# Kernel optimization log

Measured on AMD Instinct MI355X. Metric: run time of the kernel, lower is better.

## Reference

```python
import jax, jax.numpy as jnp
import numpy as np

# Complete K-ary forest: B trees, depth D levels, BFS node numbering per tree.
B, K, D = 64, 4, 6
V, L = 600, 256
N_PER = (K ** D - 1) // (K - 1)   # 1365 nodes per tree
N = B * N_PER                      # 87360 total nodes


def _schedule():
    """Per-(depth, sibling_index) groups, mirroring the torch decode_train loop
    for a complete K-ary forest. Returns list of (d, s, node_idx, parent_idx)."""
    starts = [(K ** d - 1) // (K - 1) for d in range(D)]  # level offsets within a tree
    tree_off = np.arange(B)[:, None] * N_PER
    groups = []
    for d in range(D):
        for s in (range(1) if d == 0 else range(K)):
            if d == 0:
                p = np.arange(1)                      # root
                par = None
            else:
                p = np.arange(K ** (d - 1)) * K + s   # positions with sib_pos == s
                par = (tree_off + starts[d - 1] + (p // K)[None, :]).reshape(-1)
            idx = (tree_off + starts[d] + p[None, :]).reshape(-1)
            groups.append((d, s, jnp.asarray(idx),
                           None if par is None else jnp.asarray(par)))
    return groups

GROUPS = _schedule()


def _lstm(gx, h, c, W_hh, b_ih, b_hh):
    # torch LSTMCell, gate order i, f, g, o; gx = x @ W_ih^T precomputed.
    gates = gx + b_ih + h @ W_hh.T + b_hh
    i, f, g, o = jnp.split(gates, 4, axis=1)
    c_new = jax.nn.sigmoid(f) * c + jax.nn.sigmoid(i) * jnp.tanh(g)
    return jax.nn.sigmoid(o) * jnp.tanh(c_new), c_new


def setup_inputs() -> dict:
    key = jax.random.key(0)
    ks = jax.random.split(key, 20)
    w = lambda k, shape, s=0.05: jax.random.normal(k, shape, dtype=jnp.float32) * s
    return {
        'z': w(ks[0], (B, L), 1.0),
        'features': jax.random.randint(ks[1], (N,), 0, V),
        'W_ih_p': w(ks[2], (4 * L, V)), 'W_hh_p': w(ks[3], (4 * L, L)),
        'b_ih_p': w(ks[4], (4 * L,)), 'b_hh_p': w(ks[5], (4 * L,)),
        'W_ih_s': w(ks[6], (4 * L, V)), 'W_hh_s': w(ks[7], (4 * L, L)),
        'b_ih_s': w(ks[8], (4 * L,)), 'b_hh_s': w(ks[9], (4 * L,)),
        'U_parent': w(ks[10], (L, L)), 'U_sibling': w(ks[11], (L, L)),
        'W_label': w(ks[12], (V, L)), 'b_label': w(ks[13], (V,)),
        'W_depth': w(ks[14], (1, L)), 'b_depth': w(ks[15], (1,)),
        'W_width': w(ks[16], (1, L)), 'b_width': w(ks[17], (1,)),
        'w_off_p': w(ks[18], (1, 1), 1.0), 'w_off_s': w(ks[19], (1, 1), 1.0),
    }


def reference(z, features, W_ih_p, W_hh_p, b_ih_p, b_hh_p,
              W_ih_s, W_hh_s, b_ih_s, b_hh_s, U_parent, U_sibling,
              W_label, b_label, W_depth, b_depth, W_width, b_width,
              w_off_p, w_off_s):
    h_p = jnp.zeros((N, L), jnp.float32)
    c_p = jnp.zeros((N, L), jnp.float32)
    h_s = jnp.zeros((N, L), jnp.float32)
    c_s = jnp.zeros((N, L), jnp.float32)
    pred_labels = jnp.zeros((N, V), jnp.float32)
    pred_is_parent = jnp.zeros((N,), jnp.float32)
    pred_has_sib = jnp.zeros((N,), jnp.float32)

    for d, s, idx, pidx in GROUPS:
        G = idx.shape[0]
        if d == 0:
            h_par, c_par = z, jnp.zeros((B, L), jnp.float32)
        else:
            h_par, c_par = h_p[pidx], c_p[pidx]
        if s == 0:
            h_prev = jnp.zeros((G, L), jnp.float32)
            c_prev = jnp.zeros((G, L), jnp.float32)
        else:
            h_prev, c_prev = h_s[idx - 1], c_s[idx - 1]
        # group-constant teacher flags for a complete K-ary tree
        is_par = 1.0 if d < D - 1 else 0.0
        has_sib = 1.0 if (d > 0 and s < K - 1) else 0.0

        h_pred = jnp.tanh(h_par @ U_parent.T + h_prev @ U_sibling.T)
        logits = h_pred @ W_label.T + b_label
        p_par = jax.nn.sigmoid(h_pred @ W_depth.T + b_depth)[:, 0]
        p_sib = jax.nn.sigmoid(h_pred @ W_width.T + b_width)[:, 0]
        logp = jax.nn.log_softmax(
            logits + w_off_p[0, 0] * is_par + w_off_s[0, 0] * has_sib, axis=1)

        lab = features[idx]
        gx_p = jnp.take(W_ih_p, lab, axis=1).T  # one-hot @ W_ih^T as a gather
        gx_s = jnp.take(W_ih_s, lab, axis=1).T
        hp_new, cp_new = _lstm(gx_p, h_par, c_par, W_hh_p, b_ih_p, b_hh_p)
        hs_new, cs_new = _lstm(gx_s, h_prev, c_prev, W_hh_s, b_ih_s, b_hh_s)

        h_p = h_p.at[idx].set(hp_new)
        c_p = c_p.at[idx].set(cp_new)
        h_s = h_s.at[idx].set(hs_new)
        c_s = c_s.at[idx].set(cs_new)
        pred_labels = pred_labels.at[idx].set(logp)
        pred_is_parent = pred_is_parent.at[idx].set(p_par)
        pred_has_sib = pred_has_sib.at[idx].set(p_sib)

    # pack [N, V+2]: log-softmax labels, p(is_parent), p(has_sibling)
    return jnp.concatenate(
        [pred_labels, pred_is_parent[:, None], pred_has_sib[:, None]], axis=1)
```

## Files before the change

### kernel.cpp

```cpp
#include <hip/hip_runtime.h>


typedef unsigned short u16;
typedef short bf16x8 __attribute__((ext_vector_type(8)));
typedef float f32x4 __attribute__((ext_vector_type(4)));

#define NPER 1365
#define VDIM 600
#define VD2  602

#define MODE_PPA   0
#define MODE_UPROJ 1
#define MODE_ROOT  2

__device__ __forceinline__ float b2f(u16 h) {
  union { unsigned u; float f; } v; v.u = ((unsigned)h) << 16; return v.f;
}
__device__ __forceinline__ u16 f2bf(float f) {
  union { float f; unsigned u; } v; v.f = f;
  unsigned r = v.u + 0x7fff + ((v.u >> 16) & 1);
  return (u16)(r >> 16);
}
__device__ __forceinline__ float fsigm(float x) {
  return __fdividef(1.f, 1.f + __expf(-x));
}
__device__ __forceinline__ float ftanh(float x) {
  float e = __expf(-2.f * fabsf(x));
  float r = __fdividef(1.f - e, 1.f + e);
  return x < 0.f ? -r : r;
}

__device__ __forceinline__ void ladder(int r, int& off, int& pcs, int& start) {
  if (r < 64)        { off = 0;    pcs = 0; start = 1;   }
  else if (r < 320)  { off = 64;   pcs = 2; start = 5;   }
  else if (r < 1344) { off = 320;  pcs = 4; start = 21;  }
  else if (r < 5440) { off = 1344; pcs = 6; start = 85;  }
  else               { off = 5440; pcs = 8; start = 341; }
}

__global__ void k_pack(
    const float* __restrict__ Upar, const float* __restrict__ Whhp,
    const float* __restrict__ Usib, const float* __restrict__ Whhs,
    const float* __restrict__ z, const float* __restrict__ Wihp,
    const float* __restrict__ Wihs, const float* __restrict__ Wlab,
    const float* __restrict__ Wd, const float* __restrict__ Ww,
    const float* __restrict__ blab, const float* __restrict__ bd,
    const float* __restrict__ bw, const float* __restrict__ bihp,
    const float* __restrict__ bhhp, const float* __restrict__ bihs,
    const float* __restrict__ bhhs,
    u16* __restrict__ UPWHHP, u16* __restrict__ USWHHS, u16* __restrict__ ZBF,
    u16* __restrict__ WIHPT, u16* __restrict__ WIHST, u16* __restrict__ WEXT,
    float* __restrict__ BE, float* __restrict__ BP, float* __restrict__ BS) {
  int i = blockIdx.x * 256 + threadIdx.x;
  if (i < 327680) {
    int r = i >> 8, c = i & 255;
    UPWHHP[i] = f2bf(r < 256 ? Upar[(r << 8) | c] : Whhp[((r - 256) << 8) | c]);
    return;
  }
  i -= 327680;
  if (i < 327680) {
    int r = i >> 8, c = i & 255;
    USWHHS[i] = f2bf(r < 256 ? Usib[(r << 8) | c] : Whhs[((r - 256) << 8) | c]);
    return;
  }
  i -= 327680;
  if (i < 16384) { ZBF[i] = f2bf(z[i]); return; }
  i -= 16384;
  if (i < 614400) {
    int r = i >> 10, c = i & 1023;
    WIHPT[i] = f2bf(Wihp[c * VDIM + r]); return;
  }
  i -= 614400;
  if (i < 614400) {
    int r = i >> 10, c = i & 1023;
    WIHST[i] = f2bf(Wihs[c * VDIM + r]); return;
  }
  i -= 614400;
  if (i < VD2 * 256) {
    int r = i >> 8, c = i & 255;
    float v = (r < VDIM) ? Wlab[r * 256 + c] : ((r == VDIM) ? Wd[c] : Ww[c]);
    WEXT[i] = f2bf(v); return;
  }
  i -= VD2 * 256;
  if (i < VD2) { BE[i] = (i < VDIM) ? blab[i] : ((i == VDIM) ? bd[0] : bw[0]); return; }
  i -= VD2;
  if (i < 1024) { BP[i] = bihp[i] + bhhp[i]; return; }
  i -= 1024;
  if (i < 1024) { BS[i] = bihs[i] + bhhs[i]; return; }
}

__device__ __forceinline__ void dev_dual(
    int tile, int nx, const u16* __restrict__ A, const u16* __restrict__ B,
    int M, int mode, u16* __restrict__ ppa, int ppoff,
    float* __restrict__ uproj, u16* __restrict__ gates,
    u16* __restrict__ hpred) {
  static __shared__ __align__(16) u16 As[128 * 40];
  static __shared__ __align__(16) u16 Bs[128 * 40];
  const int m0 = (tile % nx) * 128, n0 = (tile / nx) * 128;
  const int tid = threadIdx.x;
  const int wave = tid >> 6, lane = tid & 63;
  const int quad = lane >> 4, lr = lane & 15;
  const int wm = (wave >> 1) * 64, wn = (wave & 1) * 64;
  const int srow = tid >> 2;
  const int sch = (tid & 3) << 3;

  f32x4 acc[4][4] = {};
  for (int t = 0; t < 8; ++t) {
    const int kk = t * 32;
    bf16x8 a0 = *(const bf16x8*)(A + (size_t)(m0 + srow) * 256 + kk + sch);
    bf16x8 a1 = *(const bf16x8*)(A + (size_t)(m0 + srow + 64) * 256 + kk + sch);
    bf16x8 b0 = *(const bf16x8*)(B + (size_t)(n0 + srow) * 256 + kk + sch);
    bf16x8 b1 = *(const bf16x8*)(B + (size_t)(n0 + srow + 64) * 256 + kk + sch);
    __syncthreads();
    *(bf16x8*)&As[srow * 40 + sch] = a0;
    *(bf16x8*)&As[(srow + 64) * 40 + sch] = a1;
    *(bf16x8*)&Bs[srow * 40 + sch] = b0;
    *(bf16x8*)&Bs[(srow + 64) * 40 + sch] = b1;
    __syncthreads();
    bf16x8 af[4], bfr[4];
#pragma unroll
    for (int tm = 0; tm < 4; ++tm)
      af[tm] = *(const bf16x8*)&As[(wm + tm * 16 + lr) * 40 + quad * 8];
#pragma unroll
    for (int tn = 0; tn < 4; ++tn)
      bfr[tn] = *(const bf16x8*)&Bs[(wn + tn * 16 + lr) * 40 + quad * 8];
#pragma unroll
    for (int tm = 0; tm < 4; ++tm)
#pragma unroll
      for (int tn = 0; tn < 4; ++tn)
        acc[tm][tn] = __builtin_amdgcn_mfma_f32_16x16x32_bf16(
            af[tm], bfr[tn], acc[tm][tn], 0, 0, 0);
  }

  const bool isg = (n0 >= 256);
#pragma unroll
  for (int tn = 0; tn < 4; ++tn) {
    int col = n0 + wn + tn * 16 + lr;
#pragma unroll
    for (int tm = 0; tm < 4; ++tm) {
#pragma unroll
      for (int r = 0; r < 4; ++r) {
        int row = m0 + wm + tm * 16 + quad * 4 + r;
        if (row >= M) continue;
        float v = acc[tm][tn][r];
        if (isg) {
          gates[(size_t)row * 1024 + (col - 256)] = f2bf(v);
        } else if (mode == MODE_PPA) {
          ppa[(size_t)(ppoff + row) * 256 + col] = f2bf(v);
        } else if (mode == MODE_UPROJ) {
          uproj[(size_t)row * 256 + col] = v;
        } else {
          hpred[(size_t)row * NPER * 256 + col] = f2bf(ftanh(v));
        }
      }
    }
  }
}


__device__ __forceinline__ void dev_s0(int r, const u16* __restrict__ wihT,
    const float* __restrict__ bias, const int* __restrict__ feat,
    u16* __restrict__ h, u16* __restrict__ c) {
  int u = threadIdx.x;
  int off, pcs, start; ladder(r, off, pcs, start);
  int lg = r - off;
  int t = lg >> pcs, j = lg & ((1 << pcs) - 1);
  int lab = feat[t * NPER + start + 4 * j];
  const u16* wr = wihT + lab * 1024;
  float gi = b2f(wr[u])       + bias[u];
  float gg = b2f(wr[512 + u]) + bias[512 + u];
  float go = b2f(wr[768 + u]) + bias[768 + u];
  float cn = fsigm(gi) * ftanh(gg);
  float hn = fsigm(go) * ftanh(cn);
  h[(size_t)r * 256 + u] = f2bf(hn);
  c[(size_t)r * 256 + u] = f2bf(cn);
}

__device__ __forceinline__ void dev_lstm_sib(int r, int k,
    const u16* __restrict__ gates, const u16* __restrict__ wihT,
    const float* __restrict__ bias, const u16* __restrict__ c_in,
    const int* __restrict__ feat, u16* __restrict__ h, u16* __restrict__ c) {
  int u = threadIdx.x;
  int off, pcs, start; ladder(r, off, pcs, start);
  int lg = r - off;
  int t = lg >> pcs, j = lg & ((1 << pcs) - 1);
  int lab = feat[t * NPER + start + 4 * j + k];
  const u16* wr = wihT + lab * 1024;
  const u16* gr = gates + (size_t)r * 1024;
  float gi = b2f(wr[u])       + bias[u]       + b2f(gr[u]);
  float gf = b2f(wr[256 + u]) + bias[256 + u] + b2f(gr[256 + u]);
  float gg = b2f(wr[512 + u]) + bias[512 + u] + b2f(gr[512 + u]);
  float go = b2f(wr[768 + u]) + bias[768 + u] + b2f(gr[768 + u]);
  float cv = b2f(c_in[(size_t)r * 256 + u]);
  float cn = fsigm(gf) * cv + fsigm(gi) * ftanh(gg);
  float hn = fsigm(go) * ftanh(cn);
  h[(size_t)r * 256 + u] = f2bf(hn);
  c[(size_t)r * 256 + u] = f2bf(cn);
}

__device__ __forceinline__ void dev_lstm_par(int g,
    const u16* __restrict__ gates, const u16* __restrict__ wihT,
    const float* __restrict__ bias, const u16* __restrict__ c_in,
    const int* __restrict__ feat, u16* __restrict__ h, u16* __restrict__ c,
    int lsbits, int start) {
  int u = threadIdx.x;
  int t = g >> lsbits, p = g & ((1 << lsbits) - 1);
  int pr = lsbits ? ((t << (lsbits - 2)) | (p >> 2)) : g;
  int lab = feat[t * NPER + start + p];
  const u16* wr = wihT + lab * 1024;
  const u16* gr = gates + (size_t)pr * 1024;
  float gi = b2f(wr[u])       + bias[u]       + b2f(gr[u]);
  float gf = b2f(wr[256 + u]) + bias[256 + u] + b2f(gr[256 + u]);
  float gg = b2f(wr[512 + u]) + bias[512 + u] + b2f(gr[512 + u]);
  float go = b2f(wr[768 + u]) + bias[768 + u] + b2f(gr[768 + u]);
  float cv = c_in ? b2f(c_in[(size_t)pr * 256 + u]) : 0.f;
  float cn = fsigm(gf) * cv + fsigm(gi) * ftanh(gg);
  float hn = fsigm(go) * ftanh(cn);
  h[(size_t)g * 256 + u] = f2bf(hn);
  c[(size_t)g * 256 + u] = f2bf(cn);
}

__device__ __forceinline__ void dev_assemble(int r,
    const u16* __restrict__ PPA, const float* __restrict__ U1,
    const float* __restrict__ U2, const float* __restrict__ U3,
    u16* __restrict__ HPRED) {
  int u = threadIdx.x;
  int off, pcs, start; ladder(r, off, pcs, start);
  int lg = r - off;
  int t = lg >> pcs, j = lg & ((1 << pcs) - 1);
  size_t base = ((size_t)(t * NPER + start + 4 * j)) * 256 + u;
  size_t ro = (size_t)r * 256 + u;
  float pp = b2f(PPA[ro]);
  HPRED[base]       = f2bf(ftanh(pp));
  HPRED[base + 256] = f2bf(ftanh(pp + U1[ro]));
  HPRED[base + 512] = f2bf(ftanh(pp + U2[ro]));
  HPRED[base + 768] = f2bf(ftanh(pp + U3[ro]));
}


__global__ __launch_bounds__(256) void k_s0(
    const u16* WIHST, const float* BS, const int* feat, u16* h, u16* c) {
  dev_s0(blockIdx.x, WIHST, BS, feat, h, c);
}

__global__ __launch_bounds__(256) void k_gg(
    int nA,
    const u16* Aa, const u16* Ba, int Ma, int nxa, int modea,
    u16* ppaa, int ppoffa, float* uproja, u16* gatesa, u16* hpreda,
    const u16* Ab, const u16* Bb, int Mb, int nxb, int modeb,
    u16* ppab, int ppoffb, float* uprojb, u16* gatesb, u16* hpredb) {
  int b = blockIdx.x;
  if (b < nA)
    dev_dual(b, nxa, Aa, Ba, Ma, modea, ppaa, ppoffa, uproja, gatesa, hpreda);
  else
    dev_dual(b - nA, nxb, Ab, Bb, Mb, modeb, ppab, ppoffb, uprojb, gatesb,
             hpredb);
}

__global__ __launch_bounds__(256) void k_gemm(
    const u16* A, const u16* B, int M, int nx, int mode,
    u16* ppa, int ppoff, float* uproj, u16* gates, u16* hpred) {
  dev_dual(blockIdx.x, nx, A, B, M, mode, ppa, ppoff, uproj, gates, hpred);
}

__global__ __launch_bounds__(256) void k_ll(
    int nP,
    const u16* gatesP, const u16* WIHPT, const float* BP, const u16* cpin,
    u16* hpout, u16* cpout, int lsbits, int startp,
    int kS, const u16* gatesS, const u16* WIHST, const float* BS,
    const u16* csin, u16* hsout, u16* csout, const int* feat) {
  int b = blockIdx.x;
  if (b < nP)
    dev_lstm_par(b, gatesP, WIHPT, BP, cpin, feat, hpout, cpout, lsbits,
                 startp);
  else
    dev_lstm_sib(b - nP, kS, gatesS, WIHST, BS, csin, feat, hsout, csout);
}

__global__ __launch_bounds__(256) void k_plstm(
    const u16* gatesP, const u16* WIHPT, const float* BP, const u16* cpin,
    const int* feat, u16* hpout, u16* cpout, int lsbits, int start) {
  dev_lstm_par(blockIdx.x, gatesP, WIHPT, BP, cpin, feat, hpout, cpout,
               lsbits, start);
}

__global__ __launch_bounds__(256) void k_plstm_asm(
    const u16* gatesP, const u16* WIHPT, const float* BP, const u16* cpin,
    const int* feat, u16* hpout, u16* cpout,
    const u16* PPA, const float* U1, const float* U2, const float* U3,
    u16* HPRED) {
  int b = blockIdx.x;
  if (b < 16384)
    dev_lstm_par(b, gatesP, WIHPT, BP, cpin, feat, hpout, cpout, 8, 85);
  else
    dev_assemble(b - 16384, PPA, U1, U2, U3, HPRED);
}

__global__ __launch_bounds__(256) void k_assemble(
    const u16* PPA, const float* U1, const float* U2, const float* U3,
    u16* HPRED) {
  dev_assemble(5440 + blockIdx.x, PPA, U1, U2, U3, HPRED);
}

__global__ __launch_bounds__(512, 4) void k_mm_tail(
    const u16* __restrict__ A, const u16* __restrict__ B,
    const float* __restrict__ bias, float* __restrict__ out) {
  __shared__ __align__(16) u16 As[32 * 264];
  __shared__ float smax[32][8], ssum[32][8], slz[32];
  const int m0 = blockIdx.x * 32;
  const int tid = threadIdx.x;
  const int wave = tid >> 6, lane = tid & 63;
  const int quad = lane >> 4, lr = lane & 15;
  const int c0 = wave * 80;

#pragma unroll
  for (int c = 0; c < 2; ++c) {
    int idx = c * 512 + tid;
    int row = idx >> 5, ch = (idx & 31) << 3;
    *(bf16x8*)&As[row * 264 + ch] =
        *(const bf16x8*)(A + (size_t)(m0 + row) * 256 + ch);
  }
  __syncthreads();

  f32x4 acc[2][5] = {};
#pragma unroll
  for (int t = 0; t < 8; ++t) {
    bf16x8 af[2], bfr[5];
#pragma unroll
    for (int tm = 0; tm < 2; ++tm)
      af[tm] = *(const bf16x8*)&As[(tm * 16 + lr) * 264 + t * 32 + quad * 8];
#pragma unroll
    for (int tn = 0; tn < 5; ++tn)
      bfr[tn] = *(const bf16x8*)(B + (size_t)(c0 + tn * 16 + lr) * 256 +
                                 t * 32 + quad * 8);
#pragma unroll
    for (int tm = 0; tm < 2; ++tm)
#pragma unroll
      for (int tn = 0; tn < 5; ++tn)
        acc[tm][tn] = __builtin_amdgcn_mfma_f32_16x16x32_bf16(
            af[tm], bfr[tn], acc[tm][tn], 0, 0, 0);
  }

  float bv[5]; bool val[5];
#pragma unroll
  for (int tn = 0; tn < 5; ++tn) {
    int col = c0 + tn * 16 + lr;
    val[tn] = (col < VDIM);
    bv[tn] = (col < VD2) ? bias[col] : 0.f;
  }

#pragma unroll
  for (int tm = 0; tm < 2; ++tm) {
#pragma unroll
    for (int r = 0; r < 4; ++r) {
      float mx = -1e30f;
#pragma unroll
      for (int tn = 0; tn < 5; ++tn)
        if (val[tn]) mx = fmaxf(mx, acc[tm][tn][r] + bv[tn]);
#pragma unroll
      for (int o = 1; o < 16; o <<= 1) mx = fmaxf(mx, __shfl_xor(mx, o, 64));
      if (lr == 0) smax[tm * 16 + quad * 4 + r][wave] = mx;
    }
  }
  __syncthreads();
#pragma unroll
  for (int tm = 0; tm < 2; ++tm) {
#pragma unroll
    for (int r = 0; r < 4; ++r) {
      int row = tm * 16 + quad * 4 + r;
      float fm = smax[row][0];
#pragma unroll
      for (int wv = 1; wv < 8; ++wv) fm = fmaxf(fm, smax[row][wv]);
      float se = 0.f;
#pragma unroll
      for (int tn = 0; tn < 5; ++tn)
        if (val[tn]) se += __expf(acc[tm][tn][r] + bv[tn] - fm);
#pragma unroll
      for (int o = 1; o < 16; o <<= 1) se += __shfl_xor(se, o, 64);
      if (lr == 0) ssum[row][wave] = se;
    }
  }
  __syncthreads();
  if (tid < 32) {
    float fm = smax[tid][0];
#pragma unroll
    for (int wv = 1; wv < 8; ++wv) fm = fmaxf(fm, smax[tid][wv]);
    float ss = 0.f;
#pragma unroll
    for (int wv = 0; wv < 8; ++wv) ss += ssum[tid][wv];
    slz[tid] = fm + __logf(ss);
  }
  __syncthreads();

#pragma unroll
  for (int tm = 0; tm < 2; ++tm) {
#pragma unroll
    for (int tn = 0; tn < 5; ++tn) {
      int col = c0 + tn * 16 + lr;
      if (col >= VD2) continue;
#pragma unroll
      for (int r = 0; r < 4; ++r) {
        int row = tm * 16 + quad * 4 + r;
        float v = acc[tm][tn][r] + bv[tn];
        out[(size_t)(m0 + row) * VD2 + col] =
            (col < VDIM) ? (v - slz[row]) : fsigm(v);
      }
    }
  }
}


extern "C" void kernel_launch(void* const* d_in, const int* in_sizes, int n_in,
                              void* d_out, int out_size, void* d_ws, size_t ws_size,
                              hipStream_t stream) {
  const float* z    = (const float*)d_in[0];
  const int*   feat = (const int*)d_in[1];
  const float* Wihp = (const float*)d_in[2];
  const float* Whhp = (const float*)d_in[3];
  const float* bihp = (const float*)d_in[4];
  const float* bhhp = (const float*)d_in[5];
  const float* Wihs = (const float*)d_in[6];
  const float* Whhs = (const float*)d_in[7];
  const float* bihs = (const float*)d_in[8];
  const float* bhhs = (const float*)d_in[9];
  const float* Upar = (const float*)d_in[10];
  const float* Usib = (const float*)d_in[11];
  const float* Wlab = (const float*)d_in[12];
  const float* blab = (const float*)d_in[13];
  const float* Wd   = (const float*)d_in[14];
  const float* bd   = (const float*)d_in[15];
  const float* Ww   = (const float*)d_in[16];
  const float* bw   = (const float*)d_in[17];
  float* out = (float*)d_out;

  char* w = (char*)d_ws;
  auto alloc = [&](size_t bytes) {
    char* p = w; w += (bytes + 255) & ~(size_t)255; return p;
  };
  u16*   UPWHHP = (u16*)alloc((size_t)1280 * 256 * 2);
  u16*   USWHHS = (u16*)alloc((size_t)1280 * 256 * 2);
  u16*   ZBF    = (u16*)alloc((size_t)128 * 256 * 2);
  u16*   WIHPT  = (u16*)alloc((size_t)VDIM * 1024 * 2);
  u16*   WIHST  = (u16*)alloc((size_t)VDIM * 1024 * 2);
  u16*   WEXT   = (u16*)alloc((size_t)640 * 256 * 2);
  float* BE     = (float*)alloc(VD2 * 4);
  float* BP     = (float*)alloc(1024 * 4);
  float* BS     = (float*)alloc(1024 * 4);
  const size_t CR = 21888;
  u16*   HSA[3], *CSA[3];
  for (int k = 0; k < 3; ++k) {
    HSA[k] = (u16*)alloc(CR * 256 * 2);
    CSA[k] = (u16*)alloc(CR * 256 * 2);
  }
  float* UPROJ[3];
  for (int k = 0; k < 3; ++k) UPROJ[k] = (float*)alloc(CR * 256 * 4);
  u16*   PPA   = (u16*)alloc(CR * 256 * 2);
  const size_t SB = (size_t)16384 * 256 * 2;
  u16* HP[2] = {(u16*)alloc(SB), (u16*)alloc(SB)};
  u16* CP[2] = {(u16*)alloc(SB), (u16*)alloc(SB)};
  u16*   GATES  = (u16*)alloc(CR * 1024 * 2);
  u16*   GATESP = (u16*)alloc((size_t)4096 * 1024 * 2);
  u16*   HPRED  = (u16*)alloc((size_t)87424 * 256 * 2);

  k_pack<<<8037, 256, 0, stream>>>(Upar, Whhp, Usib, Whhs, z, Wihp, Wihs,
                                   Wlab, Wd, Ww, blab, bd, bw, bihp, bhhp,
                                   bihs, bhhs, UPWHHP, USWHHS, ZBF, WIHPT,
                                   WIHST, WEXT, BE, BP, BS);
  k_s0<<<21824, 256, 0, stream>>>(WIHST, BS, feat, HSA[0], CSA[0]);
  k_gg<<<10 + 1710, 256, 0, stream>>>(
      10,
      ZBF, UPWHHP, 64, 1, MODE_ROOT, nullptr, 0, nullptr, GATESP, HPRED,
      HSA[0], USWHHS, 21824, 171, MODE_UPROJ, nullptr, 0, UPROJ[0], GATES,
      nullptr);
  k_ll<<<64 + 21824, 256, 0, stream>>>(
      64, GATESP, WIHPT, BP, nullptr, HP[0], CP[0], 0, 0,
      1, GATES, WIHST, BS, CSA[0], HSA[1], CSA[1], feat);
  k_gg<<<10 + 1710, 256, 0, stream>>>(
      10,
      HP[0], UPWHHP, 64, 1, MODE_PPA, PPA, 0, nullptr, GATESP, nullptr,
      HSA[1], USWHHS, 21824, 171, MODE_UPROJ, nullptr, 0, UPROJ[1], GATES,
      nullptr);
  k_ll<<<256 + 21824, 256, 0, stream>>>(
      256, GATESP, WIHPT, BP, CP[0], HP[1], CP[1], 2, 1,
      2, GATES, WIHST, BS, CSA[1], HSA[2], CSA[2], feat);
  k_gg<<<20 + 342, 256, 0, stream>>>(
      20,
      HP[1], UPWHHP, 256, 2, MODE_PPA, PPA, 64, nullptr, GATESP, nullptr,
      HSA[2], USWHHS, 21824, 171, MODE_UPROJ, nullptr, 0, UPROJ[2], nullptr,
      nullptr);
  k_plstm<<<1024, 256, 0, stream>>>(GATESP, WIHPT, BP, CP[1], feat,
                                    HP[0], CP[0], 4, 5);
  k_gemm<<<80, 256, 0, stream>>>(HP[0], UPWHHP, 1024, 8, MODE_PPA,
                                 PPA, 320, nullptr, GATESP, nullptr);
  k_plstm<<<4096, 256, 0, stream>>>(GATESP, WIHPT, BP, CP[0], feat,
                                    HP[1], CP[1], 6, 21);
  k_gemm<<<320, 256, 0, stream>>>(HP[1], UPWHHP, 4096, 32, MODE_PPA,
                                  PPA, 1344, nullptr, GATESP, nullptr);
  k_plstm_asm<<<16384 + 5440, 256, 0, stream>>>(
      GATESP, WIHPT, BP, CP[1], feat, HP[0], CP[0],
      PPA, UPROJ[0], UPROJ[1], UPROJ[2], HPRED);
  k_gemm<<<256, 256, 0, stream>>>(HP[0], UPWHHP, 16384, 128, MODE_PPA,
                                  PPA, 5440, nullptr, nullptr, nullptr);
  k_assemble<<<16384, 256, 0, stream>>>(PPA, UPROJ[0], UPROJ[1], UPROJ[2],
                                        HPRED);
  k_mm_tail<<<2730, 512, 0, stream>>>(HPRED, WEXT, BE, out);

  (void)in_sizes; (void)n_in; (void)out_size; (void)ws_size;
}
```

Baseline: 603.3 us.

## Split weight packing, fuse s0 into packing, spread assemble across parent LSTM launches

Splits the weight-packing kernel in two. The W_ih transposes now go through a 32x32 shared-memory tile, so reads and writes are both coalesced. The remaining packing work is merged into the same launch as the sibling-0 LSTM step, and the assemble blocks for each depth range are attached to the earlier parent-LSTM launches instead of running mostly at the end. The goal is fewer launches, more coalesced transposes, and filling small parent-LSTM grids with independent assemble work, at the cost of more complex block-index dispatch.

```diff
diff --git a/kernel.cpp b/kernel.cpp
--- a/kernel.cpp
+++ b/kernel.cpp
@@ -38,123 +38,41 @@
   else               { off = 5440; pcs = 8; start = 341; }
 }
 
-__global__ void k_pack(
-    const float* __restrict__ Upar, const float* __restrict__ Whhp,
-    const float* __restrict__ Usib, const float* __restrict__ Whhs,
-    const float* __restrict__ z, const float* __restrict__ Wihp,
-    const float* __restrict__ Wihs, const float* __restrict__ Wlab,
-    const float* __restrict__ Wd, const float* __restrict__ Ww,
-    const float* __restrict__ blab, const float* __restrict__ bd,
-    const float* __restrict__ bw, const float* __restrict__ bihp,
-    const float* __restrict__ bhhp, const float* __restrict__ bihs,
-    const float* __restrict__ bhhs,
-    u16* __restrict__ UPWHHP, u16* __restrict__ USWHHS, u16* __restrict__ ZBF,
-    u16* __restrict__ WIHPT, u16* __restrict__ WIHST, u16* __restrict__ WEXT,
-    float* __restrict__ BE, float* __restrict__ BP, float* __restrict__ BS) {
-  int i = blockIdx.x * 256 + threadIdx.x;
-  if (i < 327680) {
-    int r = i >> 8, c = i & 255;
-    UPWHHP[i] = f2bf(r < 256 ? Upar[(r << 8) | c] : Whhp[((r - 256) << 8) | c]);
+__global__ __launch_bounds__(256) void k_packA(
+    const float* __restrict__ Wihp, const float* __restrict__ Wihs,
+    const float* __restrict__ bihp, const float* __restrict__ bhhp,
+    const float* __restrict__ bihs, const float* __restrict__ bhhs,
+    u16* __restrict__ WIHPT, u16* __restrict__ WIHST,
+    float* __restrict__ BP, float* __restrict__ BS) {
+  int b = blockIdx.x;
+  if (b < 1216) {
+    __shared__ u16 tile[32][34];
+    int m = (b >= 608);
+    const float* src = m ? Wihs : Wihp;
+    u16* dst = m ? WIHST : WIHPT;
+    int tb = m ? b - 608 : b;
+    int rt = tb >> 5, ct = tb & 31;
+    int r0 = rt * 32, c0 = ct * 32;
+    int tx = threadIdx.x & 31, ty = threadIdx.x >> 5;
+#pragma unroll
+    for (int yy = 0; yy < 32; yy += 8) {
+      int c = c0 + ty + yy;
+      int r = r0 + tx;
+      if (r < VDIM) tile[ty + yy][tx] = f2bf(src[(size_t)c * VDIM + r]);
+    }
+    __syncthreads();
+#pragma unroll
+    for (int yy = 0; yy < 32; yy += 8) {
+      int r = r0 + ty + yy;
+      int c = c0 + tx;
+      if (r < VDIM) dst[(size_t)r * 1024 + c] = tile[tx][ty + yy];
+    }
     return;
   }
-  i -= 327680;
-  if (i < 327680) {
-    int r = i >> 8, c = i & 255;
-    USWHHS[i] = f2bf(r < 256 ? Usib[(r << 8) | c] : Whhs[((r - 256) << 8) | c]);
-    return;
-  }
-  i -= 327680;
-  if (i < 16384) { ZBF[i] = f2bf(z[i]); return; }
-  i -= 16384;
-  if (i < 614400) {
-    int r = i >> 10, c = i & 1023;
-    WIHPT[i] = f2bf(Wihp[c * VDIM + r]); return;
-  }
-  i -= 614400;
-  if (i < 614400) {
-    int r = i >> 10, c = i & 1023;
-    WIHST[i] = f2bf(Wihs[c * VDIM + r]); return;
-  }
-  i -= 614400;
-  if (i < VD2 * 256) {
-    int r = i >> 8, c = i & 255;
-    float v = (r < VDIM) ? Wlab[r * 256 + c] : ((r == VDIM) ? Wd[c] : Ww[c]);
-    WEXT[i] = f2bf(v); return;
-  }
-  i -= VD2 * 256;
-  if (i < VD2) { BE[i] = (i < VDIM) ? blab[i] : ((i == VDIM) ? bd[0] : bw[0]); return; }
-  i -= VD2;
+  int i = (b - 1216) * 256 + threadIdx.x;
   if (i < 1024) { BP[i] = bihp[i] + bhhp[i]; return; }
   i -= 1024;
-  if (i < 1024) { BS[i] = bihs[i] + bhhs[i]; return; }
-}
-
-__device__ __forceinline__ void dev_dual(
-    int tile, int nx, const u16* __restrict__ A, const u16* __restrict__ B,
-    int M, int mode, u16* __restrict__ ppa, int ppoff,
-    float* __restrict__ uproj, u16* __restrict__ gates,
-    u16* __restrict__ hpred) {
-  static __shared__ __align__(16) u16 As[128 * 40];
-  static __shared__ __align__(16) u16 Bs[128 * 40];
-  const int m0 = (tile % nx) * 128, n0 = (tile / nx) * 128;
-  const int tid = threadIdx.x;
-  const int wave = tid >> 6, lane = tid & 63;
-  const int quad = lane >> 4, lr = lane & 15;
-  const int wm = (wave >> 1) * 64, wn = (wave & 1) * 64;
-  const int srow = tid >> 2;
-  const int sch = (tid & 3) << 3;
-
-  f32x4 acc[4][4] = {};
-  for (int t = 0; t < 8; ++t) {
-    const int kk = t * 32;
-    bf16x8 a0 = *(const bf16x8*)(A + (size_t)(m0 + srow) * 256 + kk + sch);
-    bf16x8 a1 = *(const bf16x8*)(A + (size_t)(m0 + srow + 64) * 256 + kk + sch);
-    bf16x8 b0 = *(const bf16x8*)(B + (size_t)(n0 + srow) * 256 + kk + sch);
-    bf16x8 b1 = *(const bf16x8*)(B + (size_t)(n0 + srow + 64) * 256 + kk + sch);
-    __syncthreads();
-    *(bf16x8*)&As[srow * 40 + sch] = a0;
-    *(bf16x8*)&As[(srow + 64) * 40 + sch] = a1;
-    *(bf16x8*)&Bs[srow * 40 + sch] = b0;
-    *(bf16x8*)&Bs[(srow + 64) * 40 + sch] = b1;
-    __syncthreads();
-    bf16x8 af[4], bfr[4];
-#pragma unroll
-    for (int tm = 0; tm < 4; ++tm)
-      af[tm] = *(const bf16x8*)&As[(wm + tm * 16 + lr) * 40 + quad * 8];
-#pragma unroll
-    for (int tn = 0; tn < 4; ++tn)
-      bfr[tn] = *(const bf16x8*)&Bs[(wn + tn * 16 + lr) * 40 + quad * 8];
-#pragma unroll
-    for (int tm = 0; tm < 4; ++tm)
-#pragma unroll
-      for (int tn = 0; tn < 4; ++tn)
-        acc[tm][tn] = __builtin_amdgcn_mfma_f32_16x16x32_bf16(
-            af[tm], bfr[tn], acc[tm][tn], 0, 0, 0);
-  }
-
-  const bool isg = (n0 >= 256);
-#pragma unroll
-  for (int tn = 0; tn < 4; ++tn) {
-    int col = n0 + wn + tn * 16 + lr;
-#pragma unroll
-    for (int tm = 0; tm < 4; ++tm) {
-#pragma unroll
-      for (int r = 0; r < 4; ++r) {
-        int row = m0 + wm + tm * 16 + quad * 4 + r;
-        if (row >= M) continue;
-        float v = acc[tm][tn][r];
-        if (isg) {
-          gates[(size_t)row * 1024 + (col - 256)] = f2bf(v);
-        } else if (mode == MODE_PPA) {
-          ppa[(size_t)(ppoff + row) * 256 + col] = f2bf(v);
-        } else if (mode == MODE_UPROJ) {
-          uproj[(size_t)row * 256 + col] = v;
-        } else {
-          hpred[(size_t)row * NPER * 256 + col] = f2bf(ftanh(v));
-        }
-      }
-    }
-  }
+  if (i < 1024) BS[i] = bihs[i] + bhhs[i];
 }
 
 
@@ -174,6 +92,111 @@
   float hn = fsigm(go) * ftanh(cn);
   h[(size_t)r * 256 + u] = f2bf(hn);
   c[(size_t)r * 256 + u] = f2bf(cn);
+}
+
+__global__ __launch_bounds__(256) void k_packB_s0(
+    const float* __restrict__ Upar, const float* __restrict__ Whhp,
+    const float* __restrict__ Usib, const float* __restrict__ Whhs,
+    const float* __restrict__ z, const float* __restrict__ Wlab,
+    const float* __restrict__ Wd, const float* __restrict__ Ww,
+    const float* __restrict__ blab, const float* __restrict__ bd,
+    const float* __restrict__ bw,
+    u16* __restrict__ UPWHHP, u16* __restrict__ USWHHS, u16* __restrict__ ZBF,
+    u16* __restrict__ WEXT, float* __restrict__ BE,
+    const u16* __restrict__ WIHST, const float* __restrict__ BS,
+    const int* __restrict__ feat, u16* __restrict__ h0, u16* __restrict__ c0) {
+  int b = blockIdx.x;
+  if (b < 21824) { dev_s0(b, WIHST, BS, feat, h0, c0); return; }
+  int i = (b - 21824) * 256 + threadIdx.x;
+  if (i < 327680) {
+    int r = i >> 8, c = i & 255;
+    UPWHHP[i] = f2bf(r < 256 ? Upar[(r << 8) | c] : Whhp[((r - 256) << 8) | c]);
+    return;
+  }
+  i -= 327680;
+  if (i < 327680) {
+    int r = i >> 8, c = i & 255;
+    USWHHS[i] = f2bf(r < 256 ? Usib[(r << 8) | c] : Whhs[((r - 256) << 8) | c]);
+    return;
+  }
+  i -= 327680;
+  if (i < 16384) { ZBF[i] = f2bf(z[i]); return; }
+  i -= 16384;
+  if (i < VD2 * 256) {
+    int r = i >> 8, c = i & 255;
+    float v = (r < VDIM) ? Wlab[r * 256 + c] : ((r == VDIM) ? Wd[c] : Ww[c]);
+    WEXT[i] = f2bf(v); return;
+  }
+  i -= VD2 * 256;
+  if (i < VD2) BE[i] = (i < VDIM) ? blab[i] : ((i == VDIM) ? bd[0] : bw[0]);
+}
+
+__device__ __forceinline__ void dev_dual(
+    int tile, int nx, const u16* __restrict__ A, const u16* __restrict__ B,
+    int M, int mode, u16* __restrict__ ppa, int ppoff,
+    float* __restrict__ uproj, u16* __restrict__ gates,
+    u16* __restrict__ hpred) {
+  static __shared__ __align__(16) u16 As[128 * 40];
+  static __shared__ __align__(16) u16 Bs[128 * 40];
+  const int m0 = (tile % nx) * 128, n0 = (tile / nx) * 128;
+  const int tid = threadIdx.x;
+  const int wave = tid >> 6, lane = tid & 63;
+  const int quad = lane >> 4, lr = lane & 15;
+  const int wm = (wave >> 1) * 64, wn = (wave & 1) * 64;
+  const int srow = tid >> 2;
+  const int sch = (tid & 3) << 3;
+
+  f32x4 acc[4][4] = {};
+  for (int t = 0; t < 8; ++t) {
+    const int kk = t * 32;
+    bf16x8 a0 = *(const bf16x8*)(A + (size_t)(m0 + srow) * 256 + kk + sch);
+    bf16x8 a1 = *(const bf16x8*)(A + (size_t)(m0 + srow + 64) * 256 + kk + sch);
+    bf16x8 b0 = *(const bf16x8*)(B + (size_t)(n0 + srow) * 256 + kk + sch);
+    bf16x8 b1 = *(const bf16x8*)(B + (size_t)(n0 + srow + 64) * 256 + kk + sch);
+    __syncthreads();
+    *(bf16x8*)&As[srow * 40 + sch] = a0;
+    *(bf16x8*)&As[(srow + 64) * 40 + sch] = a1;
+    *(bf16x8*)&Bs[srow * 40 + sch] = b0;
+    *(bf16x8*)&Bs[(srow + 64) * 40 + sch] = b1;
+    __syncthreads();
+    bf16x8 af[4], bfr[4];
+#pragma unroll
+    for (int tm = 0; tm < 4; ++tm)
+      af[tm] = *(const bf16x8*)&As[(wm + tm * 16 + lr) * 40 + quad * 8];
+#pragma unroll
+    for (int tn = 0; tn < 4; ++tn)
+      bfr[tn] = *(const bf16x8*)&Bs[(wn + tn * 16 + lr) * 40 + quad * 8];
+#pragma unroll
+    for (int tm = 0; tm < 4; ++tm)
+#pragma unroll
+      for (int tn = 0; tn < 4; ++tn)
+        acc[tm][tn] = __builtin_amdgcn_mfma_f32_16x16x32_bf16(
+            af[tm], bfr[tn], acc[tm][tn], 0, 0, 0);
+  }
+
+  const bool isg = (n0 >= 256);
+#pragma unroll
+  for (int tn = 0; tn < 4; ++tn) {
+    int col = n0 + wn + tn * 16 + lr;
+#pragma unroll
+    for (int tm = 0; tm < 4; ++tm) {
+#pragma unroll
+      for (int r = 0; r < 4; ++r) {
+        int row = m0 + wm + tm * 16 + quad * 4 + r;
+        if (row >= M) continue;
+        float v = acc[tm][tn][r];
+        if (isg) {
+          gates[(size_t)row * 1024 + (col - 256)] = f2bf(v);
+        } else if (mode == MODE_PPA) {
+          ppa[(size_t)(ppoff + row) * 256 + col] = f2bf(v);
+        } else if (mode == MODE_UPROJ) {
+          uproj[(size_t)row * 256 + col] = v;
+        } else {
+          hpred[(size_t)row * NPER * 256 + col] = f2bf(ftanh(v));
+        }
+      }
+    }
+  }
 }
 
 __device__ __forceinline__ void dev_lstm_sib(int r, int k,
@@ -238,11 +261,6 @@
 }
 
 
-__global__ __launch_bounds__(256) void k_s0(
-    const u16* WIHST, const float* BS, const int* feat, u16* h, u16* c) {
-  dev_s0(blockIdx.x, WIHST, BS, feat, h, c);
-}
-
 __global__ __launch_bounds__(256) void k_gg(
     int nA,
     const u16* Aa, const u16* Ba, int Ma, int nxa, int modea,
@@ -277,29 +295,24 @@
     dev_lstm_sib(b - nP, kS, gatesS, WIHST, BS, csin, feat, hsout, csout);
 }
 
-__global__ __launch_bounds__(256) void k_plstm(
+__global__ __launch_bounds__(256) void k_plstm_asm(
+    int nP,
     const u16* gatesP, const u16* WIHPT, const float* BP, const u16* cpin,
-    const int* feat, u16* hpout, u16* cpout, int lsbits, int start) {
-  dev_lstm_par(blockIdx.x, gatesP, WIHPT, BP, cpin, feat, hpout, cpout,
-               lsbits, start);
-}
-
-__global__ __launch_bounds__(256) void k_plstm_asm(
-    const u16* gatesP, const u16* WIHPT, const float* BP, const u16* cpin,
-    const int* feat, u16* hpout, u16* cpout,
-    const u16* PPA, const float* U1, const float* U2, const float* U3,
-    u16* HPRED) {
+    const int* feat, u16* hpout, u16* cpout, int lsbits, int start,
+    int asmBase, const u16* PPA, const float* U1, const float* U2,
+    const float* U3, u16* HPRED) {
   int b = blockIdx.x;
-  if (b < 16384)
-    dev_lstm_par(b, gatesP, WIHPT, BP, cpin, feat, hpout, cpout, 8, 85);
+  if (b < nP)
+    dev_lstm_par(b, gatesP, WIHPT, BP, cpin, feat, hpout, cpout, lsbits,
+                 start);
   else
-    dev_assemble(b - 16384, PPA, U1, U2, U3, HPRED);
+    dev_assemble(asmBase + b - nP, PPA, U1, U2, U3, HPRED);
 }
 
 __global__ __launch_bounds__(256) void k_assemble(
-    const u16* PPA, const float* U1, const float* U2, const float* U3,
-    u16* HPRED) {
-  dev_assemble(5440 + blockIdx.x, PPA, U1, U2, U3, HPRED);
+    int asmBase, const u16* PPA, const float* U1, const float* U2,
+    const float* U3, u16* HPRED) {
+  dev_assemble(asmBase + blockIdx.x, PPA, U1, U2, U3, HPRED);
 }
 
 __global__ __launch_bounds__(512, 4) void k_mm_tail(
@@ -462,11 +475,11 @@
   u16*   GATESP = (u16*)alloc((size_t)4096 * 1024 * 2);
   u16*   HPRED  = (u16*)alloc((size_t)87424 * 256 * 2);
 
-  k_pack<<<8037, 256, 0, stream>>>(Upar, Whhp, Usib, Whhs, z, Wihp, Wihs,
-                                   Wlab, Wd, Ww, blab, bd, bw, bihp, bhhp,
-                                   bihs, bhhs, UPWHHP, USWHHS, ZBF, WIHPT,
-                                   WIHST, WEXT, BE, BP, BS);
-  k_s0<<<21824, 256, 0, stream>>>(WIHST, BS, feat, HSA[0], CSA[0]);
+  k_packA<<<1224, 256, 0, stream>>>(Wihp, Wihs, bihp, bhhp, bihs, bhhs,
+                                    WIHPT, WIHST, BP, BS);
+  k_packB_s0<<<21824 + 3229, 256, 0, stream>>>(
+      Upar, Whhp, Usib, Whhs, z, Wlab, Wd, Ww, blab, bd, bw,
+      UPWHHP, USWHHS, ZBF, WEXT, BE, WIHST, BS, feat, HSA[0], CSA[0]);
   k_gg<<<10 + 1710, 256, 0, stream>>>(
       10,
       ZBF, UPWHHP, 64, 1, MODE_ROOT, nullptr, 0, nullptr, GATESP, HPRED,
@@ -488,21 +501,23 @@
       HP[1], UPWHHP, 256, 2, MODE_PPA, PPA, 64, nullptr, GATESP, nullptr,
       HSA[2], USWHHS, 21824, 171, MODE_UPROJ, nullptr, 0, UPROJ[2], nullptr,
       nullptr);
-  k_plstm<<<1024, 256, 0, stream>>>(GATESP, WIHPT, BP, CP[1], feat,
-                                    HP[0], CP[0], 4, 5);
+  k_plstm_asm<<<1024 + 320, 256, 0, stream>>>(
+      1024, GATESP, WIHPT, BP, CP[1], feat, HP[0], CP[0], 4, 5,
+      0, PPA, UPROJ[0], UPROJ[1], UPROJ[2], HPRED);
   k_gemm<<<80, 256, 0, stream>>>(HP[0], UPWHHP, 1024, 8, MODE_PPA,
                                  PPA, 320, nullptr, GATESP, nullptr);
-  k_plstm<<<4096, 256, 0, stream>>>(GATESP, WIHPT, BP, CP[0], feat,
-                                    HP[1], CP[1], 6, 21);
+  k_plstm_asm<<<4096 + 1024, 256, 0, stream>>>(
+      4096, GATESP, WIHPT, BP, CP[0], feat, HP[1], CP[1], 6, 21,
+      320, PPA, UPROJ[0], UPROJ[1], UPROJ[2], HPRED);
   k_gemm<<<320, 256, 0, stream>>>(HP[1], UPWHHP, 4096, 32, MODE_PPA,
                                   PPA, 1344, nullptr, GATESP, nullptr);
-  k_plstm_asm<<<16384 + 5440, 256, 0, stream>>>(
-      GATESP, WIHPT, BP, CP[1], feat, HP[0], CP[0],
-      PPA, UPROJ[0], UPROJ[1], UPROJ[2], HPRED);
+  k_plstm_asm<<<16384 + 4096, 256, 0, stream>>>(
+      16384, GATESP, WIHPT, BP, CP[1], feat, HP[0], CP[0], 8, 85,
+      1344, PPA, UPROJ[0], UPROJ[1], UPROJ[2], HPRED);
   k_gemm<<<256, 256, 0, stream>>>(HP[0], UPWHHP, 16384, 128, MODE_PPA,
                                   PPA, 5440, nullptr, nullptr, nullptr);
-  k_assemble<<<16384, 256, 0, stream>>>(PPA, UPROJ[0], UPROJ[1], UPROJ[2],
-                                        HPRED);
+  k_assemble<<<16384, 256, 0, stream>>>(5440, PPA, UPROJ[0], UPROJ[1],
+                                        UPROJ[2], HPRED);
   k_mm_tail<<<2730, 512, 0, stream>>>(HPRED, WEXT, BE, out);
 
   (void)in_sizes; (void)n_in; (void)out_size; (void)ws_size;
```

Measured after the change: 603.0 us (median of 2 runs). About the same (-0.1%).
